# Optimization experiments

Hardware: AMD Instinct MI355X
Metric: run time of the kernel (lower is better)

Reference implementation:

```python
import jax, jax.numpy as jnp
import numpy as np

D_MODEL = 1024
H = 16
D_K = D_MODEL // H
B, S = 2, 2048
NEG = -1e9


def setup_inputs() -> dict:
    key = jax.random.key(0)
    ks = jax.random.split(key, 8)
    scale = 1.0 / np.sqrt(D_MODEL)
    q = jax.random.normal(ks[0], (B, S, D_MODEL), dtype=jnp.float32)
    k = jax.random.normal(ks[1], (B, S, D_MODEL), dtype=jnp.float32)
    v = jax.random.normal(ks[2], (B, S, D_MODEL), dtype=jnp.float32)
    # causal 0/1 mask, broadcastable to [B, h, S, S]
    mask = jnp.tril(jnp.ones((S, S), dtype=jnp.int32))[None, None, :, :]
    w_q = jax.random.normal(ks[3], (D_MODEL, D_MODEL), dtype=jnp.float32) * scale
    w_k = jax.random.normal(ks[4], (D_MODEL, D_MODEL), dtype=jnp.float32) * scale
    w_v = jax.random.normal(ks[5], (D_MODEL, D_MODEL), dtype=jnp.float32) * scale
    w_o = jax.random.normal(ks[6], (D_MODEL, D_MODEL), dtype=jnp.float32) * scale
    return {"q": q, "k": k, "v": v, "mask": mask,
            "w_q": w_q, "w_k": w_k, "w_v": w_v, "w_o": w_o}


def reference(q, k, v, mask, w_q, w_k, w_v, w_o):
    # projections (no bias)
    def split_heads(x):
        Bn, Sn, _ = x.shape
        return x.reshape(Bn, Sn, H, D_K).transpose(0, 2, 1, 3)  # [B,h,S,d_k]

    qh = split_heads(q @ w_q)
    kh = split_heads(k @ w_k)
    vh = split_heads(v @ w_v)

    scores = jnp.einsum('bhqd,bhkd->bhqk', qh, kh) / jnp.sqrt(
        jnp.asarray(D_K, dtype=qh.dtype))
    scores = jnp.where(mask == 0, jnp.asarray(NEG, dtype=scores.dtype), scores)
    attn = jax.nn.softmax(scores, axis=-1)  # dropout rate 0.0 -> identity
    x = jnp.einsum('bhqk,bhkd->bhqd', attn, vh)  # [B,h,S,d_k]
    x = x.transpose(0, 2, 1, 3).reshape(q.shape[0], q.shape[1], D_MODEL)
    return x @ w_o
```

## Files before the change

kernel.cpp:

```cpp
#include <hip/hip_runtime.h>

#define D_MODEL 1024
#define NH 16
#define DK 64
#define BB 2
#define SS 2048
#define M_TOT (BB*SS)

typedef float f32x4 __attribute__((ext_vector_type(4)));
typedef float f32x16 __attribute__((ext_vector_type(16)));
typedef __bf16 bf16x8 __attribute__((ext_vector_type(8)));
typedef unsigned int u32;

#define QSCALE 0.1803368801f
#define DEFER_THR 11.5416f

__device__ __forceinline__ unsigned short f2bf(float f){
  unsigned int u = __float_as_uint(f);
  unsigned int r = (u + 0x7fffu + ((u >> 16) & 1u)) >> 16;
  return (unsigned short)r;
}

__device__ __forceinline__ void gload_lds16(const void* g, void* l){
  __builtin_amdgcn_global_load_lds((const __attribute__((address_space(1))) void*)g,
                                   (__attribute__((address_space(3))) void*)l,
                                   16, 0, 0);
}

__device__ __forceinline__ void swap_half(u32 a, u32 b, int hi, u32& x, u32& y){
#if __has_builtin(__builtin_amdgcn_permlane32_swap)
  typedef unsigned int uint2v __attribute__((ext_vector_type(2)));
  uint2v r = __builtin_amdgcn_permlane32_swap(a, b, false, false);
  x = r.x; y = r.y;
#else
  u32 as = __shfl_xor(a, 32);
  u32 bs = __shfl_xor(b, 32);
  x = hi ? bs : a;
  y = hi ? b  : as;
#endif
}

__global__ __launch_bounds__(256) void cvt3_bf16(const float* __restrict__ q,
                                                 const float* __restrict__ k,
                                                 const float* __restrict__ v,
                                                 unsigned short* __restrict__ qb,
                                                 unsigned short* __restrict__ kb,
                                                 unsigned short* __restrict__ vb){
  const int which = blockIdx.y;
  const float* in = (which == 0) ? q : (which == 1) ? k : v;
  unsigned short* out = (which == 0) ? qb : (which == 1) ? kb : vb;
  int i = blockIdx.x * 256 + threadIdx.x;
  float4 f = ((const float4*)in)[i];
  ushort4 o;
  o.x = f2bf(f.x); o.y = f2bf(f.y); o.z = f2bf(f.z); o.w = f2bf(f.w);
  ((ushort4*)out)[i] = o;
}

__global__ __launch_bounds__(256) void transpose_cvt4(const float* __restrict__ wq,
                                                      const float* __restrict__ wk,
                                                      const float* __restrict__ wv,
                                                      const float* __restrict__ wo,
                                                      unsigned short* __restrict__ WqkvT,
                                                      unsigned short* __restrict__ woT){
  __shared__ float tile[64][65];
  const int which = blockIdx.z;
  const float* w = (which == 0) ? wq : (which == 1) ? wk : (which == 2) ? wv : wo;
  unsigned short* wt = (which == 3) ? woT : (WqkvT + (size_t)which * 1024 * 1024);
  const int N = D_MODEL;
  const int bx = blockIdx.x * 64;
  const int by = blockIdx.y * 64;
  const int t = threadIdx.x;
  #pragma unroll
  for (int i = 0; i < 16; ++i){
    int idx = t + i * 256;
    int r = idx >> 6, c = idx & 63;
    tile[r][c] = w[(size_t)(by + r) * N + bx + c];
  }
  __syncthreads();
  #pragma unroll
  for (int i = 0; i < 16; ++i){
    int idx = t + i * 256;
    int r = idx >> 6, c = idx & 63;
    wt[(size_t)(bx + r) * N + by + c] = f2bf(tile[c][r]);
  }
}

__global__ __launch_bounds__(256) void gemm_qkv(const unsigned short* __restrict__ Aq,
                                                const unsigned short* __restrict__ Ak,
                                                const unsigned short* __restrict__ Av,
                                                const unsigned short* __restrict__ WT,
                                                unsigned short* __restrict__ Qh,
                                                unsigned short* __restrict__ Kh,
                                                unsigned short* __restrict__ VhT){
  __shared__ unsigned short Al[2][128 * 32];
  __shared__ unsigned short Bl[2][128 * 32];
  const int tid = threadIdx.x;
  const int wid = tid >> 6, lane = tid & 63;
  const int lr = lane & 15, lg = lane >> 4;
  const int wm = wid >> 1, wn = wid & 1;
  const int bm = blockIdx.x, bn = blockIdx.y;
  const int seg = bn >> 3;
  const unsigned short* A = (seg == 0) ? Aq : (seg == 1) ? Ak : Av;
  const int K = D_MODEL;

  f32x4 acc[4][4];
  #pragma unroll
  for (int i = 0; i < 4; ++i)
    #pragma unroll
    for (int j = 0; j < 4; ++j)
      acc[i][j] = (f32x4){0.f, 0.f, 0.f, 0.f};

  auto stage = [&](int buf, int kt){
    #pragma unroll
    for (int r = 0; r < 2; ++r){
      int vt = tid + r * 256;
      int row = vt >> 2, c8 = (vt & 3) * 8;
      gload_lds16(A  + (size_t)(bm * 128 + row) * K + kt * 32 + c8,
                  &Al[buf][(wid << 9) + r * 2048]);
      gload_lds16(WT + (size_t)(bn * 128 + row) * K + kt * 32 + c8,
                  &Bl[buf][(wid << 9) + r * 2048]);
    }
  };

  stage(0, 0);
  int cur = 0;
  for (int kt = 0; kt < 32; ++kt){
    __syncthreads();
    if (kt + 1 < 32) stage(cur ^ 1, kt + 1);
    bf16x8 af[4], bfr[4];
    #pragma unroll
    for (int i = 0; i < 4; ++i)
      af[i] = *(const bf16x8*)&Al[cur][(wm * 64 + i * 16 + lr) * 32 + lg * 8];
    #pragma unroll
    for (int j = 0; j < 4; ++j)
      bfr[j] = *(const bf16x8*)&Bl[cur][(wn * 64 + j * 16 + lr) * 32 + lg * 8];
    #pragma unroll
    for (int i = 0; i < 4; ++i)
      #pragma unroll
      for (int j = 0; j < 4; ++j)
        acc[i][j] = __builtin_amdgcn_mfma_f32_16x16x32_bf16(af[i], bfr[j], acc[i][j], 0, 0, 0);
    cur ^= 1;
  }

  if (seg < 2){
    unsigned short* O = (seg == 0) ? Qh : Kh;
    const float sc = (seg == 0) ? QSCALE : 1.0f;
    #pragma unroll
    for (int i = 0; i < 4; ++i){
      int row0 = bm * 128 + wm * 64 + i * 16 + lg * 4;
      #pragma unroll
      for (int j = 0; j < 4; ++j){
        int colseg = (bn & 7) * 128 + wn * 64 + j * 16 + lr;
        int h = colseg >> 6, dk = colseg & 63;
        #pragma unroll
        for (int p = 0; p < 4; ++p){
          int rowm = row0 + p;
          int b = rowm >> 11, s = rowm & 2047;
          O[((size_t)(b * NH + h) * SS + s) * DK + dk] = f2bf(acc[i][j][p] * sc);
        }
      }
    }
  } else {
    #pragma unroll
    for (int i = 0; i < 4; ++i){
      int row0 = bm * 128 + wm * 64 + i * 16 + lg * 4;
      int b = row0 >> 11, s = row0 & 2047;
      #pragma unroll
      for (int j = 0; j < 4; ++j){
        int colseg = (bn & 7) * 128 + wn * 64 + j * 16 + lr;
        int h = colseg >> 6, dk = colseg & 63;
        ushort4 o4;
        o4.x = f2bf(acc[i][j][0]); o4.y = f2bf(acc[i][j][1]);
        o4.z = f2bf(acc[i][j][2]); o4.w = f2bf(acc[i][j][3]);
        *(ushort4*)&VhT[((size_t)(b * NH + h) * DK + dk) * SS + s] = o4;
      }
    }
  }
}

__global__ __launch_bounds__(256) void gemm_o64(const unsigned short* __restrict__ A,
                                                const unsigned short* __restrict__ Bt,
                                                float* __restrict__ O){
  __shared__ unsigned short Al[2][64 * 32];
  __shared__ unsigned short Bl[2][128 * 32];
  const int tid = threadIdx.x;
  const int wid = tid >> 6, lane = tid & 63;
  const int lr = lane & 15, lg = lane >> 4;
  const int wm = wid >> 1, wn = wid & 1;
  const int bm = blockIdx.x, bn = blockIdx.y;
  const int K = D_MODEL;

  f32x4 acc[2][4];
  #pragma unroll
  for (int i = 0; i < 2; ++i)
    #pragma unroll
    for (int j = 0; j < 4; ++j)
      acc[i][j] = (f32x4){0.f, 0.f, 0.f, 0.f};

  auto stage = [&](int buf, int kt){
    {
      int row = tid >> 2, c8 = (tid & 3) * 8;
      gload_lds16(A + (size_t)(bm * 64 + row) * K + kt * 32 + c8,
                  &Al[buf][wid << 9]);
    }
    #pragma unroll
    for (int r = 0; r < 2; ++r){
      int vt = tid + r * 256;
      int row = vt >> 2, c8 = (vt & 3) * 8;
      gload_lds16(Bt + (size_t)(bn * 128 + row) * K + kt * 32 + c8,
                  &Bl[buf][(wid << 9) + r * 2048]);
    }
  };

  stage(0, 0);
  int cur = 0;
  for (int kt = 0; kt < 32; ++kt){
    __syncthreads();
    if (kt + 1 < 32) stage(cur ^ 1, kt + 1);
    bf16x8 af[2], bfr[4];
    #pragma unroll
    for (int i = 0; i < 2; ++i)
      af[i] = *(const bf16x8*)&Al[cur][(wm * 32 + i * 16 + lr) * 32 + lg * 8];
    #pragma unroll
    for (int j = 0; j < 4; ++j)
      bfr[j] = *(const bf16x8*)&Bl[cur][(wn * 64 + j * 16 + lr) * 32 + lg * 8];
    #pragma unroll
    for (int i = 0; i < 2; ++i)
      #pragma unroll
      for (int j = 0; j < 4; ++j)
        acc[i][j] = __builtin_amdgcn_mfma_f32_16x16x32_bf16(af[i], bfr[j], acc[i][j], 0, 0, 0);
    cur ^= 1;
  }

  #pragma unroll
  for (int i = 0; i < 2; ++i){
    int row0 = bm * 64 + wm * 32 + i * 16 + lg * 4;
    #pragma unroll
    for (int j = 0; j < 4; ++j){
      int col = bn * 128 + wn * 64 + j * 16 + lr;
      #pragma unroll
      for (int p = 0; p < 4; ++p)
        O[(size_t)(row0 + p) * D_MODEL + col] = acc[i][j][p];
    }
  }
}

__global__ __launch_bounds__(256) void attn_kernel(const unsigned short* __restrict__ Qh,
                                                   const unsigned short* __restrict__ Kh,
                                                   const unsigned short* __restrict__ VhT,
                                                   unsigned short* __restrict__ Oc){
  __shared__ unsigned short SL[2][4][4096];
  const int bh = blockIdx.x;
  const int px = blockIdx.y;
  const int tid = threadIdx.x, wid = tid >> 6, lane = tid & 63;
  const int ln = lane & 31, hi = lane >> 5;
  const int qh = wid & 1, pp = wid >> 1;
  const int b = bh >> 4, h = bh & 15;
  const size_t kvbase = (size_t)bh * SS * DK;

  #pragma unroll 1
  for (int segq = 0; segq < 2; ++segq){
    const int qblk = segq ? (31 - px) : px;
    const int q0 = qblk * 64 + qh * 32;
    const int Tw = 2 * qblk + qh;
    const int R = (qblk + 2) >> 1;

    const unsigned short* qp = Qh + kvbase + (size_t)(q0 + ln) * DK + hi * 8;
    bf16x8 qbv[4];
    #pragma unroll
    for (int c = 0; c < 4; ++c) qbv[c] = *(const bf16x8*)(qp + c * 16);

    f32x16 oa0 = {0,0,0,0,0,0,0,0,0,0,0,0,0,0,0,0};
    f32x16 oa1 = {0,0,0,0,0,0,0,0,0,0,0,0,0,0,0,0};
    float m = -1e30f, ls = 0.f;

    auto stage = [&](int bufb, int r){
      const int k0A = (2 * r) * 64;
      const int k0B = k0A + 64;
      const bool haveB = (2 * r + 1) <= qblk;
      #pragma unroll
      for (int i = 0; i < 2; ++i){
        const int c = i * 256 + tid;
        const int row = c >> 3;
        const int slot = (c & 7) ^ (row & 7);
        const int ldso = (i * 256 + wid * 64) * 8;
        gload_lds16(Kh  + kvbase + (size_t)(k0A + row) * DK + slot * 8, &SL[bufb][0][ldso]);
        gload_lds16(VhT + kvbase + (size_t)row * SS + k0A + slot * 8,   &SL[bufb][1][ldso]);
        if (haveB){
          gload_lds16(Kh  + kvbase + (size_t)(k0B + row) * DK + slot * 8, &SL[bufb][2][ldso]);
          gload_lds16(VhT + kvbase + (size_t)row * SS + k0B + slot * 8,   &SL[bufb][3][ldso]);
        }
      }
    };

    stage(0, 0);
    int cur = 0;
    #pragma unroll 1
    for (int r = 0; r < R; ++r){
      __syncthreads();
      if (r + 1 < R) stage(cur ^ 1, r + 1);

      const int t = 2 * r + pp;
      if (t <= qblk){
        const unsigned short* Kb = SL[cur][pp * 2];
        const unsigned short* Vb = SL[cur][pp * 2 + 1];

        f32x16 sta = {0,0,0,0,0,0,0,0,0,0,0,0,0,0,0,0};
        f32x16 stb = {0,0,0,0,0,0,0,0,0,0,0,0,0,0,0,0};
        __builtin_amdgcn_s_setprio(1);
        #pragma unroll
        for (int c = 0; c < 4; ++c){
          const int po = ((c * 2 + hi) ^ (ln & 7)) * 8;
          bf16x8 kfa = *(const bf16x8*)&Kb[ln * 64 + po];
          bf16x8 kfb = *(const bf16x8*)&Kb[(32 + ln) * 64 + po];
          sta = __builtin_amdgcn_mfma_f32_32x32x16_bf16(kfa, qbv[c], sta, 0, 0, 0);
          stb = __builtin_amdgcn_mfma_f32_32x32x16_bf16(kfb, qbv[c], stb, 0, 0, 0);
        }
        __builtin_amdgcn_s_setprio(0);

        const int ta = 2 * t, tb = 2 * t + 1;
        if (tb == Tw){
          #pragma unroll
          for (int rr = 0; rr < 16; ++rr){
            int kg = (rr & 3) + 8 * (rr >> 2) + 4 * hi;
            if (kg > ln) stb[rr] = -1e30f;
          }
        } else if (ta == Tw){
          #pragma unroll
          for (int rr = 0; rr < 16; ++rr){
            int kg = (rr & 3) + 8 * (rr >> 2) + 4 * hi;
            if (kg > ln) sta[rr] = -1e30f;
            stb[rr] = -1e30f;
          }
        }

        float tm[8];
        #pragma unroll
        for (int i = 0; i < 8; ++i)
          tm[i] = fmaxf(fmaxf(sta[2*i], sta[2*i+1]), fmaxf(stb[2*i], stb[2*i+1]));
        float mx = fmaxf(fmaxf(fmaxf(tm[0], tm[1]), fmaxf(tm[2], tm[3])),
                         fmaxf(fmaxf(tm[4], tm[5]), fmaxf(tm[6], tm[7])));
        mx = fmaxf(mx, __shfl_xor(mx, 32));

        if (__any(mx > m + DEFER_THR)){
          const float mn = fmaxf(m, mx);
          const float fac = __builtin_amdgcn_exp2f(m - mn);
          m = mn;
          ls *= fac;
          #pragma unroll
          for (int rr = 0; rr < 16; ++rr){ oa0[rr] *= fac; oa1[rr] *= fac; }
        }

        #pragma unroll
        for (int rr = 0; rr < 16; ++rr){
          sta[rr] = __builtin_amdgcn_exp2f(sta[rr] - m);
          stb[rr] = __builtin_amdgcn_exp2f(stb[rr] - m);
        }
        float sm[8];
        #pragma unroll
        for (int i = 0; i < 8; ++i)
          sm[i] = (sta[2*i] + sta[2*i+1]) + (stb[2*i] + stb[2*i+1]);
        float rsum = ((sm[0] + sm[1]) + (sm[2] + sm[3])) + ((sm[4] + sm[5]) + (sm[6] + sm[7]));
        rsum += __shfl_xor(rsum, 32);
        ls += rsum;

        u32 ca[8], cb[8];
        #pragma unroll
        for (int i = 0; i < 8; ++i){
          asm("v_cvt_pk_bf16_f32 %0, %1, %2" : "=v"(ca[i]) : "v"(sta[2*i]), "v"(sta[2*i+1]));
          asm("v_cvt_pk_bf16_f32 %0, %1, %2" : "=v"(cb[i]) : "v"(stb[2*i]), "v"(stb[2*i+1]));
        }
        u32 w0[4], w1[4], w2[4], w3[4];
        swap_half(ca[0], ca[2], hi, w0[0], w0[2]);
        swap_half(ca[1], ca[3], hi, w0[1], w0[3]);
        swap_half(ca[4], ca[6], hi, w1[0], w1[2]);
        swap_half(ca[5], ca[7], hi, w1[1], w1[3]);
        swap_half(cb[0], cb[2], hi, w2[0], w2[2]);
        swap_half(cb[1], cb[3], hi, w2[1], w2[3]);
        swap_half(cb[4], cb[6], hi, w3[0], w3[2]);
        swap_half(cb[5], cb[7], hi, w3[1], w3[3]);
        bf16x8 pf[4];
        __builtin_memcpy(&pf[0], w0, 16);
        __builtin_memcpy(&pf[1], w1, 16);
        __builtin_memcpy(&pf[2], w2, 16);
        __builtin_memcpy(&pf[3], w3, 16);

        __builtin_amdgcn_s_setprio(1);
        #pragma unroll
        for (int ks = 0; ks < 4; ++ks){
          const int po = ((ks * 2 + hi) ^ (ln & 7)) * 8;
          bf16x8 v0 = *(const bf16x8*)&Vb[ln * 64 + po];
          bf16x8 v1 = *(const bf16x8*)&Vb[(32 + ln) * 64 + po];
          oa0 = __builtin_amdgcn_mfma_f32_32x32x16_bf16(v0, pf[ks], oa0, 0, 0, 0);
          oa1 = __builtin_amdgcn_mfma_f32_32x32x16_bf16(v1, pf[ks], oa1, 0, 0, 0);
        }
        __builtin_amdgcn_s_setprio(0);
      }
      cur ^= 1;
    }
    __syncthreads();

    float* oL  = (float*)&SL[0][0][0];
    float* mLs = (float*)&SL[0][2][0];
    if (wid >= 2){
      const int w = wid - 2;
      #pragma unroll
      for (int rr = 0; rr < 16; ++rr){
        oL[(w * 32 + rr) * 64 + lane]      = oa0[rr];
        oL[(w * 32 + 16 + rr) * 64 + lane] = oa1[rr];
      }
      if (hi == 0){ mLs[w * 32 + ln] = m; mLs[64 + w * 32 + ln] = ls; }
    }
    __syncthreads();
    if (wid < 2){
      const float m1  = mLs[wid * 32 + ln];
      const float ls1 = mLs[64 + wid * 32 + ln];
      const float mstar = fmaxf(m, m1);
      const float f0 = __builtin_amdgcn_exp2f(m  - mstar);
      const float f1 = __builtin_amdgcn_exp2f(m1 - mstar);
      const float inv = 1.0f / (f0 * ls + f1 * ls1);
      const size_t rowbase = ((size_t)b * SS + q0 + ln) * D_MODEL + h * DK;
      #pragma unroll
      for (int g = 0; g < 4; ++g){
        ushort4 o4;
        o4.x = f2bf((f0 * oa0[4*g + 0] + f1 * oL[(wid * 32 + 4*g + 0) * 64 + lane]) * inv);
        o4.y = f2bf((f0 * oa0[4*g + 1] + f1 * oL[(wid * 32 + 4*g + 1) * 64 + lane]) * inv);
        o4.z = f2bf((f0 * oa0[4*g + 2] + f1 * oL[(wid * 32 + 4*g + 2) * 64 + lane]) * inv);
        o4.w = f2bf((f0 * oa0[4*g + 3] + f1 * oL[(wid * 32 + 4*g + 3) * 64 + lane]) * inv);
        *(ushort4*)&Oc[rowbase + 8*g + 4*hi] = o4;
      }
      #pragma unroll
      for (int g = 0; g < 4; ++g){
        ushort4 o4;
        o4.x = f2bf((f0 * oa1[4*g + 0] + f1 * oL[(wid * 32 + 16 + 4*g + 0) * 64 + lane]) * inv);
        o4.y = f2bf((f0 * oa1[4*g + 1] + f1 * oL[(wid * 32 + 16 + 4*g + 1) * 64 + lane]) * inv);
        o4.z = f2bf((f0 * oa1[4*g + 2] + f1 * oL[(wid * 32 + 16 + 4*g + 2) * 64 + lane]) * inv);
        o4.w = f2bf((f0 * oa1[4*g + 3] + f1 * oL[(wid * 32 + 16 + 4*g + 3) * 64 + lane]) * inv);
        *(ushort4*)&Oc[rowbase + 32 + 8*g + 4*hi] = o4;
      }
    }
    __syncthreads();
  }
}

extern "C" void kernel_launch(void* const* d_in, const int* in_sizes, int n_in,
                              void* d_out, int out_size, void* d_ws, size_t ws_size,
                              hipStream_t stream){
  const float* q  = (const float*)d_in[0];
  const float* k  = (const float*)d_in[1];
  const float* v  = (const float*)d_in[2];
  const float* wq = (const float*)d_in[4];
  const float* wk = (const float*)d_in[5];
  const float* wv = (const float*)d_in[6];
  const float* wo = (const float*)d_in[7];
  float* out = (float*)d_out;

  char* ws = (char*)d_ws;
  const size_t MB = 1024 * 1024;
  unsigned short* qb     = (unsigned short*)(ws + 0 * MB);
  unsigned short* kb     = (unsigned short*)(ws + 8 * MB);
  unsigned short* vb     = (unsigned short*)(ws + 16 * MB);
  unsigned short* WqkvT  = (unsigned short*)(ws + 24 * MB);
  unsigned short* woT    = (unsigned short*)(ws + 30 * MB);
  unsigned short* Qh     = (unsigned short*)(ws + 32 * MB);
  unsigned short* Kh     = (unsigned short*)(ws + 40 * MB);
  unsigned short* VhT    = (unsigned short*)(ws + 48 * MB);
  unsigned short* attnb  = (unsigned short*)(ws + 56 * MB);

  const int n4 = (M_TOT * D_MODEL) / 4;
  dim3 gc(n4 / 256, 3);
  cvt3_bf16<<<gc, 256, 0, stream>>>(q, k, v, qb, kb, vb);

  dim3 tg(16, 16, 4);
  transpose_cvt4<<<tg, 256, 0, stream>>>(wq, wk, wv, wo, WqkvT, woT);

  dim3 gqkv(M_TOT / 128, 3 * D_MODEL / 128);
  gemm_qkv<<<gqkv, 256, 0, stream>>>(qb, kb, vb, WqkvT, Qh, Kh, VhT);

  dim3 ga(BB * NH, SS / 128);
  attn_kernel<<<ga, 256, 0, stream>>>(Qh, Kh, VhT, attnb);

  dim3 go(M_TOT / 64, D_MODEL / 128);
  gemm_o64<<<go, 256, 0, stream>>>(attnb, woT, out);
}
```

Measured before the change: 122.7 us.

## Fuse fp32-to-bf16 input conversion into QKV GEMM A-tile loading

Removes the separate cvt3_bf16 kernel and has gemm_qkv stage fp32 activations directly into LDS. An XOR swizzle on the LDS layout avoids bank conflicts, and v_cvt_pk_bf16_f32 converts fragments to bf16 just before the MFMA. This saves one launch and the write and re-read of the bf16 copies of q, k and v. In exchange the GEMM loads twice as many A bytes per tile (fp32), uses more LDS and does the conversion repeatedly, once for each of the 8 column blocks that read the same A rows.

```diff
diff --git a/kernel.cpp b/kernel.cpp
--- a/kernel.cpp
+++ b/kernel.cpp
@@ -38,22 +38,6 @@
   x = hi ? bs : a;
   y = hi ? b  : as;
 #endif
-}
-
-__global__ __launch_bounds__(256) void cvt3_bf16(const float* __restrict__ q,
-                                                 const float* __restrict__ k,
-                                                 const float* __restrict__ v,
-                                                 unsigned short* __restrict__ qb,
-                                                 unsigned short* __restrict__ kb,
-                                                 unsigned short* __restrict__ vb){
-  const int which = blockIdx.y;
-  const float* in = (which == 0) ? q : (which == 1) ? k : v;
-  unsigned short* out = (which == 0) ? qb : (which == 1) ? kb : vb;
-  int i = blockIdx.x * 256 + threadIdx.x;
-  float4 f = ((const float4*)in)[i];
-  ushort4 o;
-  o.x = f2bf(f.x); o.y = f2bf(f.y); o.z = f2bf(f.z); o.w = f2bf(f.w);
-  ((ushort4*)out)[i] = o;
 }
 
 __global__ __launch_bounds__(256) void transpose_cvt4(const float* __restrict__ wq,
@@ -85,14 +69,14 @@
   }
 }
 
-__global__ __launch_bounds__(256) void gemm_qkv(const unsigned short* __restrict__ Aq,
-                                                const unsigned short* __restrict__ Ak,
-                                                const unsigned short* __restrict__ Av,
+__global__ __launch_bounds__(256) void gemm_qkv(const float* __restrict__ Aq,
+                                                const float* __restrict__ Ak,
+                                                const float* __restrict__ Av,
                                                 const unsigned short* __restrict__ WT,
                                                 unsigned short* __restrict__ Qh,
                                                 unsigned short* __restrict__ Kh,
                                                 unsigned short* __restrict__ VhT){
-  __shared__ unsigned short Al[2][128 * 32];
+  __shared__ float          Af[2][128 * 32];
   __shared__ unsigned short Bl[2][128 * 32];
   const int tid = threadIdx.x;
   const int wid = tid >> 6, lane = tid & 63;
@@ -100,7 +84,7 @@
   const int wm = wid >> 1, wn = wid & 1;
   const int bm = blockIdx.x, bn = blockIdx.y;
   const int seg = bn >> 3;
-  const unsigned short* A = (seg == 0) ? Aq : (seg == 1) ? Ak : Av;
+  const float* A = (seg == 0) ? Aq : (seg == 1) ? Ak : Av;
   const int K = D_MODEL;
 
   f32x4 acc[4][4];
@@ -110,15 +94,24 @@
     for (int j = 0; j < 4; ++j)
       acc[i][j] = (f32x4){0.f, 0.f, 0.f, 0.f};
 
+  const int lr8 = lane >> 3;
+  const int lc8 = lane & 7;
+  const int ls8 = lc8 ^ lr8;
+
   auto stage = [&](int buf, int kt){
     #pragma unroll
-    for (int r = 0; r < 2; ++r){
-      int vt = tid + r * 256;
+    for (int i = 0; i < 4; ++i){
+      const int g = wid * 4 + i;
+      const int r = g * 8 + lr8;
+      gload_lds16(A + (size_t)(bm * 128 + r) * K + kt * 32 + ls8 * 4,
+                  &Af[buf][g * 256]);
+    }
+    #pragma unroll
+    for (int rr = 0; rr < 2; ++rr){
+      int vt = tid + rr * 256;
       int row = vt >> 2, c8 = (vt & 3) * 8;
-      gload_lds16(A  + (size_t)(bm * 128 + row) * K + kt * 32 + c8,
-                  &Al[buf][(wid << 9) + r * 2048]);
       gload_lds16(WT + (size_t)(bn * 128 + row) * K + kt * 32 + c8,
-                  &Bl[buf][(wid << 9) + r * 2048]);
+                  &Bl[buf][(wid << 9) + rr * 2048]);
     }
   };
 
@@ -128,9 +121,19 @@
     __syncthreads();
     if (kt + 1 < 32) stage(cur ^ 1, kt + 1);
     bf16x8 af[4], bfr[4];
-    #pragma unroll
-    for (int i = 0; i < 4; ++i)
-      af[i] = *(const bf16x8*)&Al[cur][(wm * 64 + i * 16 + lr) * 32 + lg * 8];
+    const int rs = lr & 7;
+    #pragma unroll
+    for (int i = 0; i < 4; ++i){
+      const int row = wm * 64 + i * 16 + lr;
+      f32x4 a0 = *(const f32x4*)&Af[cur][row * 32 + (((2 * lg)     ^ rs) * 4)];
+      f32x4 a1 = *(const f32x4*)&Af[cur][row * 32 + (((2 * lg + 1) ^ rs) * 4)];
+      u32 cc[4];
+      asm("v_cvt_pk_bf16_f32 %0, %1, %2" : "=v"(cc[0]) : "v"(a0[0]), "v"(a0[1]));
+      asm("v_cvt_pk_bf16_f32 %0, %1, %2" : "=v"(cc[1]) : "v"(a0[2]), "v"(a0[3]));
+      asm("v_cvt_pk_bf16_f32 %0, %1, %2" : "=v"(cc[2]) : "v"(a1[0]), "v"(a1[1]));
+      asm("v_cvt_pk_bf16_f32 %0, %1, %2" : "=v"(cc[3]) : "v"(a1[2]), "v"(a1[3]));
+      __builtin_memcpy(&af[i], cc, 16);
+    }
     #pragma unroll
     for (int j = 0; j < 4; ++j)
       bfr[j] = *(const bf16x8*)&Bl[cur][(wn * 64 + j * 16 + lr) * 32 + lg * 8];
@@ -457,25 +460,18 @@
 
   char* ws = (char*)d_ws;
   const size_t MB = 1024 * 1024;
-  unsigned short* qb     = (unsigned short*)(ws + 0 * MB);
-  unsigned short* kb     = (unsigned short*)(ws + 8 * MB);
-  unsigned short* vb     = (unsigned short*)(ws + 16 * MB);
-  unsigned short* WqkvT  = (unsigned short*)(ws + 24 * MB);
-  unsigned short* woT    = (unsigned short*)(ws + 30 * MB);
-  unsigned short* Qh     = (unsigned short*)(ws + 32 * MB);
-  unsigned short* Kh     = (unsigned short*)(ws + 40 * MB);
-  unsigned short* VhT    = (unsigned short*)(ws + 48 * MB);
-  unsigned short* attnb  = (unsigned short*)(ws + 56 * MB);
-
-  const int n4 = (M_TOT * D_MODEL) / 4;
-  dim3 gc(n4 / 256, 3);
-  cvt3_bf16<<<gc, 256, 0, stream>>>(q, k, v, qb, kb, vb);
+  unsigned short* WqkvT  = (unsigned short*)(ws + 0 * MB);
+  unsigned short* woT    = (unsigned short*)(ws + 6 * MB);
+  unsigned short* Qh     = (unsigned short*)(ws + 8 * MB);
+  unsigned short* Kh     = (unsigned short*)(ws + 16 * MB);
+  unsigned short* VhT    = (unsigned short*)(ws + 24 * MB);
+  unsigned short* attnb  = (unsigned short*)(ws + 32 * MB);
 
   dim3 tg(16, 16, 4);
   transpose_cvt4<<<tg, 256, 0, stream>>>(wq, wk, wv, wo, WqkvT, woT);
 
   dim3 gqkv(M_TOT / 128, 3 * D_MODEL / 128);
-  gemm_qkv<<<gqkv, 256, 0, stream>>>(qb, kb, vb, WqkvT, Qh, Kh, VhT);
+  gemm_qkv<<<gqkv, 256, 0, stream>>>(q, k, v, WqkvT, Qh, Kh, VhT);
 
   dim3 ga(BB * NH, SS / 128);
   attn_kernel<<<ga, 256, 0, stream>>>(Qh, Kh, VhT, attnb);
```

Measured after the change: 118.7 us. 3.3% less time.
